# Performance work log

Hardware: AMD Instinct MI355X
Metric: run time of the kernel (lower is better)

## Reference

```python
import jax, jax.numpy as jnp
import numpy as np

EMB = 2048
HEADS = 16
HEAD = EMB // HEADS


def setup_inputs() -> dict:
    key = jax.random.key(0)
    ks = jax.random.split(key, 10)
    B, S = 4, 2048
    x = jax.random.normal(ks[0], (B, S, EMB), dtype=jnp.float32)
    # additive causal mask: 0 on/below diagonal, -inf above
    neg_inf = jnp.finfo(jnp.float32).min
    attn_mask = jnp.where(jnp.tril(jnp.ones((S, S), dtype=bool)), 0.0, neg_inf).astype(jnp.float32)
    scale = 1.0 / np.sqrt(EMB)  # xavier-ish init scale
    Wq = jax.random.normal(ks[1], (EMB, EMB), dtype=jnp.float32) * scale
    Wk = jax.random.normal(ks[2], (EMB, EMB), dtype=jnp.float32) * scale
    Wv = jax.random.normal(ks[3], (EMB, EMB), dtype=jnp.float32) * scale
    Wo = jax.random.normal(ks[4], (EMB, EMB), dtype=jnp.float32) * scale
    bq = jnp.zeros((EMB,), dtype=jnp.float32)
    bk = jnp.zeros((EMB,), dtype=jnp.float32)
    bv = jnp.zeros((EMB,), dtype=jnp.float32)
    bo = jnp.zeros((EMB,), dtype=jnp.float32)
    return {"x": x, "attn_mask": attn_mask, "Wq": Wq, "bq": bq, "Wk": Wk, "bk": bk,
            "Wv": Wv, "bv": bv, "Wo": Wo, "bo": bo}


def reference(x, attn_mask, Wq, bq, Wk, bk, Wv, bv, Wo, bo):
    B, S, E = x.shape
    # torch Linear: y = x @ W.T + b
    def proj(W, b):
        y = jnp.einsum('bse,fe->bsf', x, W) + b
        return y.reshape(B, S, HEADS, HEAD).transpose(0, 2, 1, 3)  # [B,H,S,D]
    q = proj(Wq, bq)
    k = proj(Wk, bk)
    v = proj(Wv, bv)
    scores = jnp.einsum('bhqd,bhkd->bhqk', q, k) / np.sqrt(HEAD)
    scores = scores + attn_mask  # broadcast [S,S] over [B,H,S,S]
    attn = jax.nn.softmax(scores, axis=-1)  # dropout p=0.0 -> identity
    ctx = jnp.einsum('bhqk,bhkd->bhqd', attn, v)
    ctx = ctx.transpose(0, 2, 1, 3).reshape(B, S, E)
    out = jnp.einsum('bse,fe->bsf', ctx, Wo) + bo
    return out
```

## Files before the change

### kernel.cpp

```cpp
#include <hip/hip_runtime.h>

#define BATCH 4
#define SEQ   2048
#define EMBD  2048
#define NHEAD 16
#define HEADD 128

#define GM (BATCH*SEQ)
#define GN EMBD
#define GK EMBD

typedef __attribute__((ext_vector_type(8))) short short8;
typedef __attribute__((ext_vector_type(4))) short s16x4;
typedef __attribute__((ext_vector_type(4))) float f32x4;

static __device__ __forceinline__ short f2bf(float f) {
  unsigned u = __builtin_bit_cast(unsigned, f);
  unsigned r = (u + 0x7fffu + ((u >> 16) & 1u)) >> 16;
  return (short)r;
}

static __device__ __forceinline__ unsigned cvt_pk_bf16(float lo, float hi) {
  unsigned r;
  asm("v_cvt_pk_bf16_f32 %0, %1, %2" : "=v"(r) : "v"(lo), "v"(hi));
  return r;
}

static __device__ __forceinline__ void glds16(const short* g, short* l) {
  __builtin_amdgcn_global_load_lds(
      (const __attribute__((address_space(1))) unsigned int*)g,
      (__attribute__((address_space(3))) unsigned int*)l, 16, 0, 0);
}

__global__ __launch_bounds__(256) void cvt_f32_bf16(
    const float* __restrict__ in, short* __restrict__ out, int n)
{
  int i = (blockIdx.x * 256 + threadIdx.x) * 8;
  if (i + 7 < n) {
    float4 a = *(const float4*)&in[i];
    float4 b = *(const float4*)&in[i + 4];
    short8 o;
    o[0] = f2bf(a.x); o[1] = f2bf(a.y); o[2] = f2bf(a.z); o[3] = f2bf(a.w);
    o[4] = f2bf(b.x); o[5] = f2bf(b.y); o[6] = f2bf(b.z); o[7] = f2bf(b.w);
    *(short8*)&out[i] = o;
  }
}

__global__ __launch_bounds__(256) void cvt_w4(
    const float* __restrict__ w0, const float* __restrict__ w1,
    const float* __restrict__ w2, const float* __restrict__ w3,
    short* __restrict__ o0, short* __restrict__ o1,
    short* __restrict__ o2, short* __restrict__ o3)
{
  const float* src = blockIdx.y == 0 ? w0 : blockIdx.y == 1 ? w1 : blockIdx.y == 2 ? w2 : w3;
  short*       dst = blockIdx.y == 0 ? o0 : blockIdx.y == 1 ? o1 : blockIdx.y == 2 ? o2 : o3;
  int i = (blockIdx.x * 256 + threadIdx.x) * 8;
  float4 a = *(const float4*)&src[i];
  float4 b = *(const float4*)&src[i + 4];
  short8 o;
  o[0] = f2bf(a.x); o[1] = f2bf(a.y); o[2] = f2bf(a.z); o[3] = f2bf(a.w);
  o[4] = f2bf(b.x); o[5] = f2bf(b.y); o[6] = f2bf(b.z); o[7] = f2bf(b.w);
  *(short8*)&dst[i] = o;
}

#define BKT 32
#define NTILES (GK / BKT)

template<bool F32OUT>
__global__ __launch_bounds__(512, 2) void gemm_bias_kernel(
    const short* __restrict__ A, const short* __restrict__ W,
    const float* __restrict__ bias, void* __restrict__ Cout)
{
  __shared__ short As[4][256 * 32];
  __shared__ short Bs[4][256 * 32];

  const int tid  = threadIdx.x;
  const int lane = tid & 63;
  const int wv   = tid >> 6;
  const int quad = lane >> 4;
  const int l15  = lane & 15;

  const int bid = blockIdx.x;
  const int swz = (bid & 7) * 32 + (bid >> 3);
  const int n0 = (swz & 7) * 256;
  const int m0 = (swz >> 3) * 256;

  const int wm0 = (wv >> 2) * 128;
  const int wn0 = (wv & 3) * 64;

  size_t aoff[2], boff[2];
#pragma unroll
  for (int j = 0; j < 2; ++j) {
    int g   = j * 512 + tid;
    int row = g >> 2;
    int cgl = (g & 3) ^ ((row & 3) ^ ((row >> 2) & 1));
    aoff[j] = (size_t)(m0 + row) * GK + cgl * 8;
    boff[j] = (size_t)(n0 + row) * GK + cgl * 8;
  }

#define GSTAGE(t_) do {                                                      \
    int buf_ = (t_) & 3; int k0_ = (t_) * BKT;                               \
    _Pragma("unroll")                                                        \
    for (int j = 0; j < 2; ++j) {                                            \
      glds16(&A[aoff[j] + k0_], &As[buf_][(j * 512 + wv * 64) * 8]);         \
      glds16(&W[boff[j] + k0_], &Bs[buf_][(j * 512 + wv * 64) * 8]);         \
    }                                                                        \
  } while (0)

  const int fsw = (l15 & 3) ^ ((l15 >> 2) & 1);
  const f32x4 zerov = {0.f, 0.f, 0.f, 0.f};
  f32x4 acc[8][4];
#pragma unroll
  for (int mi = 0; mi < 8; ++mi)
#pragma unroll
    for (int ni = 0; ni < 4; ++ni) acc[mi][ni] = zerov;

  GSTAGE(0); GSTAGE(1); GSTAGE(2);

  for (int t = 0; t < NTILES; ++t) {
    if (t + 2 < NTILES)      asm volatile("s_waitcnt vmcnt(8)" ::: "memory");
    else if (t + 1 < NTILES) asm volatile("s_waitcnt vmcnt(4)" ::: "memory");
    else                     asm volatile("s_waitcnt vmcnt(0)" ::: "memory");
    __builtin_amdgcn_sched_barrier(0);
    __builtin_amdgcn_s_barrier();
    __builtin_amdgcn_sched_barrier(0);
    if (t + 3 < NTILES) GSTAGE(t + 3);
    __builtin_amdgcn_sched_barrier(0);

    const short* ap = &As[t & 3][0];
    const short* bp = &Bs[t & 3][0];
    short8 af[8], bfr[4];
#pragma unroll
    for (int mi = 0; mi < 8; ++mi) {
      int row = wm0 + mi * 16 + l15;
      af[mi] = *(const short8*)&ap[(row * 4 + (quad ^ fsw)) * 8];
    }
#pragma unroll
    for (int ni = 0; ni < 4; ++ni) {
      int row = wn0 + ni * 16 + l15;
      bfr[ni] = *(const short8*)&bp[(row * 4 + (quad ^ fsw)) * 8];
    }
    __builtin_amdgcn_s_setprio(1);
#pragma unroll
    for (int mi = 0; mi < 8; ++mi)
#pragma unroll
      for (int ni = 0; ni < 4; ++ni)
        acc[mi][ni] = __builtin_amdgcn_mfma_f32_16x16x32_bf16(af[mi], bfr[ni], acc[mi][ni], 0, 0, 0);
    __builtin_amdgcn_s_setprio(0);
    __builtin_amdgcn_sched_barrier(0);
  }
#undef GSTAGE

#pragma unroll
  for (int mi = 0; mi < 8; ++mi) {
    int mg = m0 + wm0 + mi * 16 + quad * 4;
#pragma unroll
    for (int ni = 0; ni < 4; ++ni) {
      int ng = n0 + wn0 + ni * 16 + l15;
      float bv = bias[ng];
#pragma unroll
      for (int r = 0; r < 4; ++r) {
        float val = acc[mi][ni][r] + bv;
        if (F32OUT)
          ((float*)Cout)[(size_t)(mg + r) * GN + ng] = val;
        else
          ((short*)Cout)[(size_t)(mg + r) * GN + ng] = f2bf(val);
      }
    }
  }
}

__global__ __launch_bounds__(256) void transpose_v(
    const short* __restrict__ V, short* __restrict__ Vt)
{
  __shared__ short T[64][72];
  const int b  = blockIdx.z;
  const int n0 = blockIdx.x * 64;
  const int s0 = blockIdx.y * 64;
#pragma unroll
  for (int rr = 0; rr < 2; ++rr) {
    int c = rr * 256 + threadIdx.x;
    int srow = c >> 3;
    int ncol = (c & 7) << 3;
    *(short8*)&T[srow][ncol] = *(const short8*)&V[((size_t)b * SEQ + s0 + srow) * EMBD + n0 + ncol];
  }
  __syncthreads();
#pragma unroll
  for (int rr = 0; rr < 2; ++rr) {
    int c = rr * 256 + threadIdx.x;
    int nrow = c >> 3;
    int scol = (c & 7) << 3;
    short8 o;
#pragma unroll
    for (int j = 0; j < 8; ++j) o[j] = T[scol + j][nrow];
    *(short8*)&Vt[((size_t)b * EMBD + n0 + nrow) * SEQ + s0 + scol] = o;
  }
}

__global__ __launch_bounds__(256) void flash_attn(
    const short* __restrict__ Q, const short* __restrict__ K,
    const short* __restrict__ Vt, short* __restrict__ Ctx)
{
  __shared__ short Ksf[2][64 * 128];
  __shared__ short Vsf[2][128 * 64];
  __shared__ short Ps[4][16][72];

  const int bid  = blockIdx.x;
  const int slot = bid >> 3;
  const int grp  = ((bid & 7) << 3) | (slot >> 4);
  const int xq   = slot & 15;
  const int h = grp & 15, b = grp >> 4;

  const int tid = threadIdx.x, lane = tid & 63, wv = tid >> 6;
  const int quad = lane >> 4, l15 = lane & 15;

  const size_t bhq    = (size_t)b * SEQ * EMBD + (size_t)h * HEADD;
  const size_t vtbase = ((size_t)b * EMBD + (size_t)h * HEADD) * SEQ;
  const float SL2E = 0.08838834764831845f * 1.4426950408889634f;
  const float THRS = 8.0f / SL2E;
  const int NQT = SEQ / 64;

  int kco[4], koff[4], voff[4];
#pragma unroll
  for (int rr = 0; rr < 4; ++rr) {
    int c = rr * 4 + wv;
    int g = c * 64 + lane;
    kco[rr] = c * 512;
    { int row = g >> 4, col16 = (g & 15) ^ (row & 15);
      koff[rr] = row * EMBD + col16 * 8; }
    { int row = g >> 3, col8 = (g & 7) ^ (row & 7);
      voff[rr] = row * SEQ + col8 * 8; }
  }

#define STAGE(buf, kt_) do {                                                 \
    const short* kb_ = &K[bhq + (size_t)((kt_) * 64) * EMBD];                \
    const short* vb_ = &Vt[vtbase + (size_t)((kt_) * 64)];                   \
    _Pragma("unroll")                                                        \
    for (int rr = 0; rr < 4; ++rr) {                                         \
      glds16(&kb_[koff[rr]], &Ksf[buf][kco[rr]]);                            \
      glds16(&vb_[voff[rr]], &Vsf[buf][kco[rr]]);                            \
    }                                                                        \
  } while (0)

  const f32x4 zerov = {0.f, 0.f, 0.f, 0.f};

  for (int pass = 0; pass < 2; ++pass) {
    const int qt = pass ? (NQT - 1 - xq) : xq;
    const int qg    = qt * 64 + wv * 16 + l15;
    const int rowg0 = qt * 64 + wv * 16 + quad * 4;

    short8 qf[4];
#pragma unroll
    for (int ks = 0; ks < 4; ++ks)
      qf[ks] = *(const short8*)&Q[bhq + (size_t)qg * EMBD + ks * 32 + quad * 8];

    f32x4 oacc[8];
#pragma unroll
    for (int ni = 0; ni < 8; ++ni) oacc[ni] = zerov;
    float m_s = -INFINITY;
    float l_s = 0.f;

    __syncthreads();
    STAGE(0, 0);

    for (int kt = 0; kt <= qt; ++kt) {
      const int cur = kt & 1;
      __syncthreads();
      if (kt < qt) STAGE(cur ^ 1, kt + 1);

      f32x4 sA[4];
#pragma unroll
      for (int ni = 0; ni < 4; ++ni) sA[ni] = zerov;
#pragma unroll
      for (int ks = 0; ks < 4; ++ks)
#pragma unroll
        for (int ni = 0; ni < 4; ++ni) {
          int row = ni * 16 + l15;
          short8 kf = *(const short8*)&Ksf[cur][(row * 16 + ((ks * 4 + quad) ^ (row & 15))) * 8];
          sA[ni] = __builtin_amdgcn_mfma_f32_16x16x32_bf16(kf, qf[ks], sA[ni], 0, 0, 0);
        }

      if (kt == qt) {
        const int key00 = kt * 64;
#pragma unroll
        for (int ni = 0; ni < 4; ++ni)
#pragma unroll
          for (int r = 0; r < 4; ++r) {
            int keyg = key00 + ni * 16 + quad * 4 + r;
            if (keyg > qg) sA[ni][r] = -INFINITY;
          }
      }

      float mv = sA[0][0];
#pragma unroll
      for (int ni = 0; ni < 4; ++ni)
#pragma unroll
        for (int r = 0; r < 4; ++r)
          if (ni | r) mv = fmaxf(mv, sA[ni][r]);
      mv = fmaxf(mv, __shfl_xor(mv, 16, 64));
      mv = fmaxf(mv, __shfl_xor(mv, 32, 64));

      if (!__all(mv <= m_s + THRS)) {
        float mn = fmaxf(m_s, mv);
        float alpha = exp2f((m_s - mn) * SL2E);
        m_s = mn;
        l_s *= alpha;
        float al[4];
#pragma unroll
        for (int r = 0; r < 4; ++r) al[r] = __shfl(alpha, quad * 4 + r, 16);
#pragma unroll
        for (int ni = 0; ni < 8; ++ni)
#pragma unroll
          for (int r = 0; r < 4; ++r) oacc[ni][r] *= al[r];
      }

      float msl = m_s * SL2E;
      float sum = 0.f;
#pragma unroll
      for (int ni = 0; ni < 4; ++ni)
#pragma unroll
        for (int r = 0; r < 4; ++r) {
          float p = exp2f(sA[ni][r] * SL2E - msl);
          sA[ni][r] = p;
          sum += p;
        }
      sum += __shfl_xor(sum, 16, 64);
      sum += __shfl_xor(sum, 32, 64);
      l_s += sum;

#pragma unroll
      for (int ni = 0; ni < 4; ++ni) {
        uint2 pk;
        pk.x = cvt_pk_bf16(sA[ni][0], sA[ni][1]);
        pk.y = cvt_pk_bf16(sA[ni][2], sA[ni][3]);
        *(uint2*)&Ps[wv][l15][ni * 16 + quad * 4] = pk;
      }

      short8 pf[2];
#pragma unroll
      for (int ks = 0; ks < 2; ++ks)
        pf[ks] = *(const short8*)&Ps[wv][l15][ks * 32 + quad * 8];
#pragma unroll
      for (int ni = 0; ni < 8; ++ni)
#pragma unroll
        for (int ks = 0; ks < 2; ++ks) {
          int row = ni * 16 + l15;
          short8 vf = *(const short8*)&Vsf[cur][(row * 8 + ((ks * 4 + quad) ^ (row & 7))) * 8];
          oacc[ni] = __builtin_amdgcn_mfma_f32_16x16x32_bf16(pf[ks], vf, oacc[ni], 0, 0, 0);
        }
    }

    float linv = 1.0f / l_s;
    float iv[4];
#pragma unroll
    for (int r = 0; r < 4; ++r) iv[r] = __shfl(linv, quad * 4 + r, 16);
#pragma unroll
    for (int r = 0; r < 4; ++r)
#pragma unroll
      for (int ni = 0; ni < 8; ++ni)
        Ctx[bhq + (size_t)(rowg0 + r) * EMBD + ni * 16 + l15] = f2bf(oacc[ni][r] * iv[r]);
  }
#undef STAGE
}

extern "C" void kernel_launch(void* const* d_in, const int* in_sizes, int n_in,
                              void* d_out, int out_size, void* d_ws, size_t ws_size,
                              hipStream_t stream)
{
  const float* x  = (const float*)d_in[0];
  const float* Wq = (const float*)d_in[2];
  const float* bq = (const float*)d_in[3];
  const float* Wk = (const float*)d_in[4];
  const float* bk = (const float*)d_in[5];
  const float* Wv = (const float*)d_in[6];
  const float* bv = (const float*)d_in[7];
  const float* Wo = (const float*)d_in[8];
  const float* bo = (const float*)d_in[9];
  float* out = (float*)d_out;

  const size_t NE = (size_t)BATCH * SEQ * EMBD;
  const size_t NW = (size_t)EMBD * EMBD;
  short* xb  = (short*)d_ws;
  short* wqb = xb  + NE;
  short* wkb = wqb + NW;
  short* wvb = wkb + NW;
  short* wob = wvb + NW;
  short* q   = wob + NW;
  short* k   = q   + NE;
  short* v   = k   + NE;
  short* vt  = v   + NE;
  short* ctx = v;

  cvt_f32_bf16<<<NE / (256 * 8), 256, 0, stream>>>(x, xb, (int)NE);
  cvt_w4<<<dim3(NW / (256 * 8), 4), 256, 0, stream>>>(Wq, Wk, Wv, Wo, wqb, wkb, wvb, wob);

  dim3 gg((GM / 256) * (GN / 256));
  gemm_bias_kernel<false><<<gg, 512, 0, stream>>>(xb, wqb, bq, q);
  gemm_bias_kernel<false><<<gg, 512, 0, stream>>>(xb, wkb, bk, k);
  gemm_bias_kernel<false><<<gg, 512, 0, stream>>>(xb, wvb, bv, v);
  transpose_v<<<dim3(EMBD / 64, SEQ / 64, BATCH), 256, 0, stream>>>(v, vt);
  flash_attn<<<dim3((SEQ / 128) * NHEAD * BATCH), 256, 0, stream>>>(q, k, vt, ctx);
  gemm_bias_kernel<true><<<gg, 512, 0, stream>>>(ctx, wob, bo, out);
}
```

Measured before the change: 662.8 us.

## Restructure projection GEMM into 64-wide K tiles with four-phase interleaved load/MFMA schedule

Replaces the four-stage BK=32 pipeline in the bias GEMM with a double-buffered BK=64 scheme that splits each K tile into A/B half-tiles. Global-to-LDS loads for half-tiles are issued between four MFMA quadrant phases, so staging of upcoming data overlaps compute at finer granularity. It also switches to an 8-way XOR swizzle for the wider rows. The aim is fewer barriers per K element and better hiding of load latency, at the cost of a more intricate barrier and waitcnt schedule that is easy to get wrong.

```diff
diff --git a/kernel.cpp b/kernel.cpp
--- a/kernel.cpp
+++ b/kernel.cpp
@@ -63,51 +63,54 @@
   *(short8*)&dst[i] = o;
 }
 
-#define BKT 32
-#define NTILES (GK / BKT)
+#define NKT (GK / 64)
 
 template<bool F32OUT>
 __global__ __launch_bounds__(512, 2) void gemm_bias_kernel(
     const short* __restrict__ A, const short* __restrict__ W,
     const float* __restrict__ bias, void* __restrict__ Cout)
 {
-  __shared__ short As[4][256 * 32];
-  __shared__ short Bs[4][256 * 32];
+  __shared__ short SH[2][2][2][128 * 64];
 
   const int tid  = threadIdx.x;
   const int lane = tid & 63;
   const int wv   = tid >> 6;
   const int quad = lane >> 4;
   const int l15  = lane & 15;
+  const int rsw  = l15 & 7;
 
   const int bid = blockIdx.x;
   const int swz = (bid & 7) * 32 + (bid >> 3);
   const int n0 = (swz & 7) * 256;
   const int m0 = (swz >> 3) * 256;
 
-  const int wm0 = (wv >> 2) * 128;
-  const int wn0 = (wv & 3) * 64;
-
-  size_t aoff[2], boff[2];
+  const int hA = wv >> 2;
+  const int hB = (wv & 3) >> 1;
+  const int bl = (wv & 1) * 64;
+
+  int grow[2], gcol[2];
 #pragma unroll
   for (int j = 0; j < 2; ++j) {
-    int g   = j * 512 + tid;
-    int row = g >> 2;
-    int cgl = (g & 3) ^ ((row & 3) ^ ((row >> 2) & 1));
-    aoff[j] = (size_t)(m0 + row) * GK + cgl * 8;
-    boff[j] = (size_t)(n0 + row) * GK + cgl * 8;
-  }
-
-#define GSTAGE(t_) do {                                                      \
-    int buf_ = (t_) & 3; int k0_ = (t_) * BKT;                               \
+    int gi = j * 512 + tid;
+    int row = gi >> 3, slot = gi & 7;
+    grow[j] = row;
+    gcol[j] = (slot ^ (row & 7)) * 8;
+  }
+
+#define STG(mat_, src_, rb_, kt_, h_) do {                                   \
+    short* ld_ = &SH[(kt_) & 1][mat_][h_][0];                                \
     _Pragma("unroll")                                                        \
-    for (int j = 0; j < 2; ++j) {                                            \
-      glds16(&A[aoff[j] + k0_], &As[buf_][(j * 512 + wv * 64) * 8]);         \
-      glds16(&W[boff[j] + k0_], &Bs[buf_][(j * 512 + wv * 64) * 8]);         \
-    }                                                                        \
+    for (int j = 0; j < 2; ++j)                                              \
+      glds16(&src_[(size_t)((rb_) + (h_) * 128 + grow[j]) * GK +             \
+                   (kt_) * 64 + gcol[j]],                                    \
+             &ld_[(j * 512 + wv * 64) * 8]);                                 \
   } while (0)
 
-  const int fsw = (l15 & 3) ^ ((l15 >> 2) & 1);
+#define ARD(mi_, ks_) (*(const short8*)&Abase[                               \
+    (((mi_) * 16 + l15) * 8 + (((ks_) * 4 + quad) ^ rsw)) * 8])
+#define BRD(ni_, ks_) (*(const short8*)&Bbase[                               \
+    ((bl + (ni_) * 16 + l15) * 8 + (((ks_) * 4 + quad) ^ rsw)) * 8])
+
   const f32x4 zerov = {0.f, 0.f, 0.f, 0.f};
   f32x4 acc[8][4];
 #pragma unroll
@@ -115,42 +118,110 @@
 #pragma unroll
     for (int ni = 0; ni < 4; ++ni) acc[mi][ni] = zerov;
 
-  GSTAGE(0); GSTAGE(1); GSTAGE(2);
-
-  for (int t = 0; t < NTILES; ++t) {
-    if (t + 2 < NTILES)      asm volatile("s_waitcnt vmcnt(8)" ::: "memory");
-    else if (t + 1 < NTILES) asm volatile("s_waitcnt vmcnt(4)" ::: "memory");
-    else                     asm volatile("s_waitcnt vmcnt(0)" ::: "memory");
-    __builtin_amdgcn_sched_barrier(0);
-    __builtin_amdgcn_s_barrier();
-    __builtin_amdgcn_sched_barrier(0);
-    if (t + 3 < NTILES) GSTAGE(t + 3);
-    __builtin_amdgcn_sched_barrier(0);
-
-    const short* ap = &As[t & 3][0];
-    const short* bp = &Bs[t & 3][0];
-    short8 af[8], bfr[4];
-#pragma unroll
-    for (int mi = 0; mi < 8; ++mi) {
-      int row = wm0 + mi * 16 + l15;
-      af[mi] = *(const short8*)&ap[(row * 4 + (quad ^ fsw)) * 8];
-    }
-#pragma unroll
-    for (int ni = 0; ni < 4; ++ni) {
-      int row = wn0 + ni * 16 + l15;
-      bfr[ni] = *(const short8*)&bp[(row * 4 + (quad ^ fsw)) * 8];
-    }
+  STG(0, A, m0, 0, 0); STG(1, W, n0, 0, 0); STG(1, W, n0, 0, 1);
+  STG(0, A, m0, 0, 1);
+  STG(1, W, n0, 1, 0); STG(1, W, n0, 1, 1); STG(0, A, m0, 1, 0);
+  asm volatile("s_waitcnt vmcnt(6)" ::: "memory");
+  __builtin_amdgcn_sched_barrier(0);
+  __builtin_amdgcn_s_barrier();
+
+  for (int kt = 0; kt < NKT; ++kt) {
+    const int d = kt & 1;
+    const short* Abase = &SH[d][0][hA][0];
+    const short* Bbase = &SH[d][1][hB][0];
+    short8 afA[4][2], afB[4][2], bfA[2][2], bfB[2][2];
+
+#pragma unroll
+    for (int mi = 0; mi < 4; ++mi)
+#pragma unroll
+      for (int ks = 0; ks < 2; ++ks) afA[mi][ks] = ARD(mi, ks);
+#pragma unroll
+    for (int ni = 0; ni < 2; ++ni)
+#pragma unroll
+      for (int ks = 0; ks < 2; ++ks) bfA[ni][ks] = BRD(ni, ks);
+    if (kt + 1 < NKT) STG(0, A, m0, kt + 1, 1);
+    __builtin_amdgcn_sched_barrier(0);
+    asm volatile("s_waitcnt lgkmcnt(8)" ::: "memory");
+    __builtin_amdgcn_s_barrier();
+    asm volatile("s_waitcnt lgkmcnt(0)" ::: "memory");
+    __builtin_amdgcn_sched_barrier(0);
     __builtin_amdgcn_s_setprio(1);
 #pragma unroll
-    for (int mi = 0; mi < 8; ++mi)
-#pragma unroll
-      for (int ni = 0; ni < 4; ++ni)
-        acc[mi][ni] = __builtin_amdgcn_mfma_f32_16x16x32_bf16(af[mi], bfr[ni], acc[mi][ni], 0, 0, 0);
+    for (int mi = 0; mi < 4; ++mi)
+#pragma unroll
+      for (int ni = 0; ni < 2; ++ni)
+#pragma unroll
+        for (int ks = 0; ks < 2; ++ks)
+          acc[mi][ni] = __builtin_amdgcn_mfma_f32_16x16x32_bf16(afA[mi][ks], bfA[ni][ks], acc[mi][ni], 0, 0, 0);
     __builtin_amdgcn_s_setprio(0);
     __builtin_amdgcn_sched_barrier(0);
-  }
-#undef GSTAGE
-
+    __builtin_amdgcn_s_barrier();
+
+#pragma unroll
+    for (int ni = 0; ni < 2; ++ni)
+#pragma unroll
+      for (int ks = 0; ks < 2; ++ks) bfB[ni][ks] = BRD(ni + 2, ks);
+    __builtin_amdgcn_sched_barrier(0);
+    __builtin_amdgcn_s_barrier();
+    asm volatile("s_waitcnt lgkmcnt(0)" ::: "memory");
+    __builtin_amdgcn_sched_barrier(0);
+    __builtin_amdgcn_s_setprio(1);
+#pragma unroll
+    for (int mi = 0; mi < 4; ++mi)
+#pragma unroll
+      for (int ni = 0; ni < 2; ++ni)
+#pragma unroll
+        for (int ks = 0; ks < 2; ++ks)
+          acc[mi][ni + 2] = __builtin_amdgcn_mfma_f32_16x16x32_bf16(afA[mi][ks], bfB[ni][ks], acc[mi][ni + 2], 0, 0, 0);
+    __builtin_amdgcn_s_setprio(0);
+    __builtin_amdgcn_sched_barrier(0);
+    __builtin_amdgcn_s_barrier();
+
+#pragma unroll
+    for (int mi = 0; mi < 4; ++mi)
+#pragma unroll
+      for (int ks = 0; ks < 2; ++ks) afB[mi][ks] = ARD(mi + 4, ks);
+    if (kt + 2 < NKT) STG(1, W, n0, kt + 2, 0);
+    __builtin_amdgcn_sched_barrier(0);
+    __builtin_amdgcn_s_barrier();
+    asm volatile("s_waitcnt lgkmcnt(0)" ::: "memory");
+    __builtin_amdgcn_sched_barrier(0);
+    __builtin_amdgcn_s_setprio(1);
+#pragma unroll
+    for (int mi = 0; mi < 4; ++mi)
+#pragma unroll
+      for (int ni = 0; ni < 2; ++ni)
+#pragma unroll
+        for (int ks = 0; ks < 2; ++ks)
+          acc[mi + 4][ni] = __builtin_amdgcn_mfma_f32_16x16x32_bf16(afB[mi][ks], bfA[ni][ks], acc[mi + 4][ni], 0, 0, 0);
+    __builtin_amdgcn_s_setprio(0);
+    __builtin_amdgcn_sched_barrier(0);
+    __builtin_amdgcn_s_barrier();
+
+    if (kt + 2 < NKT) { STG(1, W, n0, kt + 2, 1); STG(0, A, m0, kt + 2, 0); }
+    if (kt + 2 < NKT)      asm volatile("s_waitcnt vmcnt(6)" ::: "memory");
+    else if (kt + 1 < NKT) asm volatile("s_waitcnt vmcnt(0)" ::: "memory");
+    __builtin_amdgcn_sched_barrier(0);
+    __builtin_amdgcn_s_barrier();
+    __builtin_amdgcn_sched_barrier(0);
+    __builtin_amdgcn_s_setprio(1);
+#pragma unroll
+    for (int mi = 0; mi < 4; ++mi)
+#pragma unroll
+      for (int ni = 0; ni < 2; ++ni)
+#pragma unroll
+        for (int ks = 0; ks < 2; ++ks)
+          acc[mi + 4][ni + 2] = __builtin_amdgcn_mfma_f32_16x16x32_bf16(afB[mi][ks], bfB[ni][ks], acc[mi + 4][ni + 2], 0, 0, 0);
+    __builtin_amdgcn_s_setprio(0);
+    __builtin_amdgcn_sched_barrier(0);
+    __builtin_amdgcn_s_barrier();
+  }
+#undef STG
+#undef ARD
+#undef BRD
+
+  const int wm0 = hA * 128;
+  const int wn0 = (wv & 3) * 64;
 #pragma unroll
   for (int mi = 0; mi < 8; ++mi) {
     int mg = m0 + wm0 + mi * 16 + quad * 4;
```

Result: faster. 571.5 us (-13.8%).
